# Optimization experiments

Hardware: AMD Instinct MI355X
Metric: run time of the kernel (lower is better)

Reference implementation:

```python
import jax, jax.numpy as jnp
import numpy as np


def _chamfer(x1, x2):
    # x1: [B,N,3], x2: [B,M,3]
    # squared pairwise distances via ||a||^2 + ||b||^2 - 2 a.b (fused, no [B,N,M,3] diff tensor)
    n1 = jnp.sum(x1 * x1, axis=-1)                     # [B,N]
    n2 = jnp.sum(x2 * x2, axis=-1)                     # [B,M]
    cross = jnp.einsum('bnd,bmd->bnm', x1, x2)         # [B,N,M]
    d = n1[:, :, None] + n2[:, None, :] - 2.0 * cross  # [B,N,M]
    d = jnp.maximum(d, 0.0)
    dist1 = jnp.min(d, axis=2)  # [B,N] nearest in x2 for each x1 point
    dist2 = jnp.min(d, axis=1)  # [B,M] nearest in x1 for each x2 point
    return dist1, dist2


def setup_inputs() -> dict:
    key = jax.random.key(0)
    k1, k2 = jax.random.split(key)
    B, N, M, D = 16, 4096, 4096, 3
    input1 = jax.random.normal(k1, (B, N, D), dtype=jnp.float32)
    input2 = jax.random.normal(k2, (B, M, D), dtype=jnp.float32)
    return {"input1": input1, "input2": input2}


def reference(input1, input2):
    return _chamfer(input1, input2)
```

## Files before the change

### kernel.cpp

```cpp
#include <hip/hip_runtime.h>


#define CB 16
#define CN 4096
#define CM 4096
#define WVS 8
#define NQT 8
#define QPW (NQT * 16)
#define TPB 1024
#define NTT (TPB / 16)
#define RECV4 3
#define ZPADV4 (TPB * RECV4)

typedef float f32x4 __attribute__((ext_vector_type(4)));
typedef short bf16x8 __attribute__((ext_vector_type(8)));
typedef unsigned int u32;
typedef u32 u32x4 __attribute__((ext_vector_type(4)));
typedef float v4f __attribute__((ext_vector_type(4)));

__device__ __forceinline__ u32 f2bf(float f) {
    u32 u = __float_as_uint(f);
    return (u + 0x7FFFu + ((u >> 16) & 1u)) >> 16;
}
__device__ __forceinline__ float bf2f(u32 h) { return __uint_as_float(h << 16); }

__global__ void init_out(unsigned* __restrict__ out)
{
    out[blockIdx.x * 512 + threadIdx.x] = 0x7F800000u;
}

__global__ __launch_bounds__(512, 4) void chamfer_mfma(
    const float* __restrict__ x1, const float* __restrict__ x2,
    unsigned* __restrict__ out)
{
    const int dir    = blockIdx.z;
    const int b      = blockIdx.y;
    const int qtile  = blockIdx.x & 3;
    const int tchunk = blockIdx.x >> 2;

    const float* __restrict__ qraw = (dir ? x2 : x1) + (size_t)b * CN * 3;
    const float* __restrict__ traw = (dir ? x1 : x2) + (size_t)b * CM * 3
                                   + (size_t)tchunk * TPB * 3;
    unsigned* __restrict__ o = out + (dir ? ((size_t)CB * CN + (size_t)b * CM)
                                          : ((size_t)b * CN)) + qtile * 1024;

    __shared__ u32x4 ldsv[TPB * RECV4 + 16];

    const int tid  = threadIdx.x;
    const int lane = tid & 63;
    const int wave = __builtin_amdgcn_readfirstlane(tid >> 6);
    const int row  = lane & 15;
    const int kb   = lane >> 4;

    if (tid < 256) {
        const v4f* rv = (const v4f*)(traw + (size_t)12 * tid);
        v4f r0 = rv[0], r1 = rv[1], r2 = rv[2];
        const float tx[4] = {r0.x, r0.w, r1.z, r2.y};
        const float ty[4] = {r0.y, r1.x, r1.w, r2.z};
        const float tz[4] = {r0.z, r1.y, r2.x, r2.w};
        #pragma unroll
        for (int i = 0; i < 4; ++i) {
            float X = tx[i], Y = ty[i], Z = tz[i];
            u32 xh = f2bf(X), yh = f2bf(Y), zh = f2bf(Z);
            u32 xl = f2bf(X - bf2f(xh));
            u32 yl = f2bf(Y - bf2f(yh));
            u32 zl = f2bf(Z - bf2f(zh));
            float nt = fmaf(X, X, fmaf(Y, Y, Z * Z));
            u32 nh = f2bf(nt), nl = f2bf(nt - bf2f(nh));
            const int r = 4 * tid + i;
            ldsv[r * RECV4 + 0] = (u32x4){xh | (yh << 16), zh | (xl << 16),
                                          yl | (zl << 16), xh | (yh << 16)};
            ldsv[r * RECV4 + 1] = (u32x4){zh | (nh << 16), nl, 0u, 0u};
        }
    }
    if (tid < 16) ldsv[ZPADV4 + tid] = (u32x4){0u, 0u, 0u, 0u};

    const int qbase = qtile * 1024 + wave * QPW;
    bf16x8 bq[NQT];
    float nq[NQT];
    #pragma unroll
    for (int qt = 0; qt < NQT; ++qt) {
        const float* qp = qraw + (size_t)3 * (qbase + qt * 16 + row);
        float qx = qp[0], qy = qp[1], qz = qp[2];
        nq[qt] = fmaf(qx, qx, fmaf(qy, qy, qz * qz));
        float MX = -2.f * qx, MY = -2.f * qy, MZ = -2.f * qz;
        u32 xh = f2bf(MX), yh = f2bf(MY), zh = f2bf(MZ);
        u32 xl = f2bf(MX - bf2f(xh));
        u32 yl = f2bf(MY - bf2f(yh));
        u32 zl = f2bf(MZ - bf2f(zh));
        u32x4 w;
        if (kb == 0)
            w = (u32x4){xh | (yh << 16), zh | (xh << 16),
                        yh | (zh << 16), xl | (yl << 16)};
        else if (kb == 1)
            w = (u32x4){zl | (0x3F80u << 16), 0x3F80u, 0u, 0u};
        else
            w = (u32x4){0u, 0u, 0u, 0u};
        bq[qt] = __builtin_bit_cast(bf16x8, w);
    }

    __syncthreads();

    u32 a_idx = (kb < 2) ? (u32)(row * RECV4 + kb) : (u32)(ZPADV4 + row);
    const u32 a_step = (kb < 2) ? (u32)(16 * RECV4) : 0u;

    float best[NQT];
    #pragma unroll
    for (int qt = 0; qt < NQT; ++qt) best[qt] = 1e30f;

    #pragma unroll 1
    for (int t = 0; t < NTT; ++t) {
        bf16x8 af = __builtin_bit_cast(bf16x8, ldsv[a_idx]);
        a_idx += a_step;
        #pragma unroll
        for (int qt = 0; qt < NQT; ++qt) {
            f32x4 acc = __builtin_amdgcn_mfma_f32_16x16x32_bf16(
                af, bq[qt], (f32x4){0.f, 0.f, 0.f, 0.f}, 0, 0, 0);
            best[qt] = fminf(fminf(best[qt], acc.x), acc.y);
            best[qt] = fminf(fminf(best[qt], acc.z), acc.w);
        }
    }

    #pragma unroll
    for (int qt = 0; qt < NQT; ++qt) {
        float v = best[qt];
        v = fminf(v, __shfl_xor(v, 16));
        v = fminf(v, __shfl_xor(v, 32));
        if (kb == 0) {
            float val = fmaxf(v + nq[qt], 0.f);
            atomicMin(o + wave * QPW + qt * 16 + row, __float_as_uint(val));
        }
    }
}

extern "C" void kernel_launch(void* const* d_in, const int* in_sizes, int n_in,
                              void* d_out, int out_size, void* d_ws, size_t ws_size,
                              hipStream_t stream) {
    const float* x1 = (const float*)d_in[0];
    const float* x2 = (const float*)d_in[1];
    unsigned* out = (unsigned*)d_out;

    init_out<<<dim3(2 * CB * CN / 512), 512, 0, stream>>>(out);
    chamfer_mfma<<<dim3(16, CB, 2), 512, 0, stream>>>(x1, x2, out);
}
```

Measured before the change: 81.67 us.

## Shrink per-wave query tiles, split target chunks finer, prefetch LDS operand

Each wave now handles 4 query tiles instead of 8, and each block handles 512 targets instead of 1024, giving 2048 blocks instead of 512, with launch bounds raised to allow 8 blocks per SM. The LDS layout is changed to a dense per-lane 64-entry slab, with the zero padding stored explicitly. Each target point is converted by one thread. The next A fragment is prefetched from LDS, and the min reduction is split into two independent chains to shorten dependency latency. The cost is more blocks, fewer MFMAs per LDS load, and twice as many atomicMin writes to the output.

```diff
diff --git a/kernel.cpp b/kernel.cpp
--- a/kernel.cpp
+++ b/kernel.cpp
@@ -5,18 +5,16 @@
 #define CN 4096
 #define CM 4096
 #define WVS 8
-#define NQT 8
+#define NQT 4
 #define QPW (NQT * 16)
-#define TPB 1024
+#define QPB (WVS * QPW)
+#define TPB 512
 #define NTT (TPB / 16)
-#define RECV4 3
-#define ZPADV4 (TPB * RECV4)
 
 typedef float f32x4 __attribute__((ext_vector_type(4)));
 typedef short bf16x8 __attribute__((ext_vector_type(8)));
 typedef unsigned int u32;
 typedef u32 u32x4 __attribute__((ext_vector_type(4)));
-typedef float v4f __attribute__((ext_vector_type(4)));
 
 __device__ __forceinline__ u32 f2bf(float f) {
     u32 u = __float_as_uint(f);
@@ -29,22 +27,22 @@
     out[blockIdx.x * 512 + threadIdx.x] = 0x7F800000u;
 }
 
-__global__ __launch_bounds__(512, 4) void chamfer_mfma(
+__global__ __launch_bounds__(512, 8) void chamfer_mfma(
     const float* __restrict__ x1, const float* __restrict__ x2,
     unsigned* __restrict__ out)
 {
     const int dir    = blockIdx.z;
     const int b      = blockIdx.y;
-    const int qtile  = blockIdx.x & 3;
-    const int tchunk = blockIdx.x >> 2;
+    const int qtile  = blockIdx.x & 7;
+    const int tchunk = blockIdx.x >> 3;
 
     const float* __restrict__ qraw = (dir ? x2 : x1) + (size_t)b * CN * 3;
     const float* __restrict__ traw = (dir ? x1 : x2) + (size_t)b * CM * 3
                                    + (size_t)tchunk * TPB * 3;
     unsigned* __restrict__ o = out + (dir ? ((size_t)CB * CN + (size_t)b * CM)
-                                          : ((size_t)b * CN)) + qtile * 1024;
+                                          : ((size_t)b * CN)) + qtile * QPB;
 
-    __shared__ u32x4 ldsv[TPB * RECV4 + 16];
+    __shared__ u32x4 AI[NTT * 64];
 
     const int tid  = threadIdx.x;
     const int lane = tid & 63;
@@ -52,35 +50,29 @@
     const int row  = lane & 15;
     const int kb   = lane >> 4;
 
-    if (tid < 256) {
-        const v4f* rv = (const v4f*)(traw + (size_t)12 * tid);
-        v4f r0 = rv[0], r1 = rv[1], r2 = rv[2];
-        const float tx[4] = {r0.x, r0.w, r1.z, r2.y};
-        const float ty[4] = {r0.y, r1.x, r1.w, r2.z};
-        const float tz[4] = {r0.z, r1.y, r2.x, r2.w};
-        #pragma unroll
-        for (int i = 0; i < 4; ++i) {
-            float X = tx[i], Y = ty[i], Z = tz[i];
-            u32 xh = f2bf(X), yh = f2bf(Y), zh = f2bf(Z);
-            u32 xl = f2bf(X - bf2f(xh));
-            u32 yl = f2bf(Y - bf2f(yh));
-            u32 zl = f2bf(Z - bf2f(zh));
-            float nt = fmaf(X, X, fmaf(Y, Y, Z * Z));
-            u32 nh = f2bf(nt), nl = f2bf(nt - bf2f(nh));
-            const int r = 4 * tid + i;
-            ldsv[r * RECV4 + 0] = (u32x4){xh | (yh << 16), zh | (xl << 16),
-                                          yl | (zl << 16), xh | (yh << 16)};
-            ldsv[r * RECV4 + 1] = (u32x4){zh | (nh << 16), nl, 0u, 0u};
-        }
+    {
+        const float* tp3 = traw + 3 * tid;
+        float X = tp3[0], Y = tp3[1], Z = tp3[2];
+        u32 xh = f2bf(X), yh = f2bf(Y), zh = f2bf(Z);
+        u32 xl = f2bf(X - bf2f(xh));
+        u32 yl = f2bf(Y - bf2f(yh));
+        u32 zl = f2bf(Z - bf2f(zh));
+        float nt = fmaf(X, X, fmaf(Y, Y, Z * Z));
+        u32 nh = f2bf(nt), nl = f2bf(nt - bf2f(nh));
+        const int base = (tid >> 4) * 64 + (tid & 15);
+        AI[base +  0] = (u32x4){xh | (yh << 16), zh | (xl << 16),
+                                yl | (zl << 16), xh | (yh << 16)};
+        AI[base + 16] = (u32x4){zh | (nh << 16), nl, 0u, 0u};
+        AI[base + 32] = (u32x4){0u, 0u, 0u, 0u};
+        AI[base + 48] = (u32x4){0u, 0u, 0u, 0u};
     }
-    if (tid < 16) ldsv[ZPADV4 + tid] = (u32x4){0u, 0u, 0u, 0u};
 
-    const int qbase = qtile * 1024 + wave * QPW;
     bf16x8 bq[NQT];
     float nq[NQT];
     #pragma unroll
     for (int qt = 0; qt < NQT; ++qt) {
-        const float* qp = qraw + (size_t)3 * (qbase + qt * 16 + row);
+        const float* qp = qraw
+            + (size_t)3 * (qtile * QPB + wave * QPW + qt * 16 + row);
         float qx = qp[0], qy = qp[1], qz = qp[2];
         nq[qt] = fmaf(qx, qx, fmaf(qy, qy, qz * qz));
         float MX = -2.f * qx, MY = -2.f * qy, MZ = -2.f * qz;
@@ -99,31 +91,30 @@
         bq[qt] = __builtin_bit_cast(bf16x8, w);
     }
 
+    float best0[NQT], best1[NQT];
+    #pragma unroll
+    for (int qt = 0; qt < NQT; ++qt) { best0[qt] = 1e30f; best1[qt] = 1e30f; }
+
     __syncthreads();
 
-    u32 a_idx = (kb < 2) ? (u32)(row * RECV4 + kb) : (u32)(ZPADV4 + row);
-    const u32 a_step = (kb < 2) ? (u32)(16 * RECV4) : 0u;
-
-    float best[NQT];
-    #pragma unroll
-    for (int qt = 0; qt < NQT; ++qt) best[qt] = 1e30f;
-
+    const u32x4* ap = &AI[lane];
+    bf16x8 af = __builtin_bit_cast(bf16x8, ap[0]);
     #pragma unroll 1
     for (int t = 0; t < NTT; ++t) {
-        bf16x8 af = __builtin_bit_cast(bf16x8, ldsv[a_idx]);
-        a_idx += a_step;
+        bf16x8 afn = __builtin_bit_cast(bf16x8, ap[((t + 1) & (NTT - 1)) * 64]);
         #pragma unroll
         for (int qt = 0; qt < NQT; ++qt) {
             f32x4 acc = __builtin_amdgcn_mfma_f32_16x16x32_bf16(
                 af, bq[qt], (f32x4){0.f, 0.f, 0.f, 0.f}, 0, 0, 0);
-            best[qt] = fminf(fminf(best[qt], acc.x), acc.y);
-            best[qt] = fminf(fminf(best[qt], acc.z), acc.w);
+            best0[qt] = fminf(fminf(best0[qt], acc.x), acc.y);
+            best1[qt] = fminf(fminf(best1[qt], acc.z), acc.w);
         }
+        af = afn;
     }
 
     #pragma unroll
     for (int qt = 0; qt < NQT; ++qt) {
-        float v = best[qt];
+        float v = fminf(best0[qt], best1[qt]);
         v = fminf(v, __shfl_xor(v, 16));
         v = fminf(v, __shfl_xor(v, 32));
         if (kb == 0) {
@@ -141,5 +132,5 @@
     unsigned* out = (unsigned*)d_out;
 
     init_out<<<dim3(2 * CB * CN / 512), 512, 0, stream>>>(out);
-    chamfer_mfma<<<dim3(16, CB, 2), 512, 0, stream>>>(x1, x2, out);
+    chamfer_mfma<<<dim3(64, CB, 2), 512, 0, stream>>>(x1, x2, out);
 }
```

Measured after the change: 80.00 us. -2.0%, faster.
